# Kernel tuning notes

Measured on AMD Instinct MI355X. Metric: run time of the kernel, lower is better.

Reference implementation:

```python
import jax, jax.numpy as jnp
import numpy as np

# 3x3 Gaussian smoothing kernel (symmetric, so correlation == convolution)
GAUSS = jnp.array([[1., 2., 1.], [2., 4., 2.], [1., 2., 1.]], dtype=jnp.float32) / 16.0


def _per_sample_conv_valid(x, k):
    """Per-sample 3x3 cross-correlation. x: [B,H,W], k: [B,3,3] -> [B,H-2,W-2].

    Implemented as a grouped conv treating batch as channels (groups=B),
    matching F.conv2d(pred.permute(1,0,2,3), weight=k[:,None], groups=B).
    """
    B = x.shape[0]
    out = jax.lax.conv_general_dilated(
        x[None],            # [1, B, H, W]
        k[:, None],         # [B, 1, 3, 3]
        window_strides=(1, 1), padding='VALID',
        dimension_numbers=('NCHW', 'OIHW', 'NCHW'),
        feature_group_count=B)
    return out[0]


def _gauss_blur_same(x):
    """SAME-padded 3x3 Gaussian smoothing. x: [B,h,w] -> [B,h,w]."""
    out = jax.lax.conv_general_dilated(
        x[:, None],                 # [B,1,h,w]
        GAUSS[None, None],          # [1,1,3,3]
        window_strides=(1, 1), padding='SAME',
        dimension_numbers=('NCHW', 'OIHW', 'NCHW'))
    return out[:, 0]


def setup_inputs() -> dict:
    key = jax.random.key(0)
    k1, k2, k3, k4 = jax.random.split(key, 4)
    B, H, W = 256, 256, 256
    pred = jax.random.normal(k1, (B, H, W), dtype=jnp.float32)
    rhs = jax.random.normal(k2, (B, H - 2, W - 2), dtype=jnp.float32)
    Laplace_kernel = jax.random.normal(k3, (B, 3, 3), dtype=jnp.float32)
    Df_dr_kernel = jax.random.normal(k4, (B, 3, 3), dtype=jnp.float32)
    RR = jnp.arange(B * H * W, dtype=jnp.float32).reshape(B, H, W)
    ZZ = jnp.arange(B * H * W, dtype=jnp.float32).reshape(B, H, W)
    return {"pred": pred, "rhs": rhs, "Laplace_kernel": Laplace_kernel,
            "Df_dr_kernel": Df_dr_kernel, "RR": RR, "ZZ": ZZ}


def reference(pred, rhs, Laplace_kernel, Df_dr_kernel, RR, ZZ):
    # Finite-difference Grad-Shafranov operator (per-sample stencils).
    Lpsi = _per_sample_conv_valid(pred, Laplace_kernel)          # [B,H-2,W-2]
    Dpsi_dr = -_per_sample_conv_valid(pred, Df_dr_kernel)        # [B,H-2,W-2]
    RR_in = RR[:, 1:-1, 1:-1]
    Dpsi_dr = Dpsi_dr / RR_in
    GS_ope = Lpsi - Dpsi_dr

    # Grid spacings and normalization alfa / (hr^2 * hz^2)
    hr = RR[:, 1, 2] - RR[:, 1, 1]                               # [B]
    hz = ZZ[:, 2, 1] - ZZ[:, 1, 1]                               # [B]
    alfa = -2.0 * (hr ** 2 + hz ** 2)
    scale = (alfa / (hr ** 2 * hz ** 2))[:, None, None]
    GS_ope = GS_ope * scale

    # Gaussian smoothing then MSE against rhs
    GS_ope = _gauss_blur_same(GS_ope)
    return jnp.mean((GS_ope - rhs) ** 2)
```

## Files before the change

kernel.cpp:

```cpp
#include <hip/hip_runtime.h>

#define HW 256
#define OW 254
#define RSTRIP 16
#define NBLOCK 1024
#define NOUT (256.0f * 254.0f * 254.0f)

__device__ __forceinline__ void load_row8(const float* __restrict__ base, int row,
                                          int cL, int c0, int cB, float* p) {
    p[0] = base[row * HW + cL];
    float4 v0 = *(const float4*)&base[row * HW + c0];
    p[1] = v0.x; p[2] = v0.y; p[3] = v0.z; p[4] = v0.w;
    float4 v1 = *(const float4*)&base[row * HW + cB];
    p[5] = v1.x; p[6] = v1.y; p[7] = v1.z;
}

__global__ __launch_bounds__(256) void pde_loss_main(
    const float* __restrict__ pred, const float* __restrict__ rhs,
    const float* __restrict__ Lk,   const float* __restrict__ Dk,
    const float* __restrict__ RR,   const float* __restrict__ ZZ,
    float* __restrict__ partial)
{
    const int tid  = threadIdx.x;
    const int lane = tid & 63;
    const int wv   = tid >> 6;
    const int gw   = blockIdx.x * 4 + wv;
    const int b    = gw >> 4;
    const int strip= gw & 15;
    const int r0   = strip * RSTRIP;
    const int r1   = min(r0 + RSTRIP, OW);

    const float* predb = pred + (size_t)b * (HW * HW);
    const float* RRb   = RR   + (size_t)b * (HW * HW);
    const float* ZZb   = ZZ   + (size_t)b * (HW * HW);
    const float* rhsb  = rhs  + (size_t)b * (OW * OW);

    float kl[9], kd[9];
    #pragma unroll
    for (int q = 0; q < 9; q++) { kl[q] = Lk[b * 9 + q]; kd[q] = Dk[b * 9 + q]; }
    float hr = RRb[1 * HW + 2] - RRb[1 * HW + 1];
    float hz = ZZb[2 * HW + 1] - ZZb[1 * HW + 1];
    float hr2 = hr * hr, hz2 = hz * hz;
    const float scale = (-2.0f * (hr2 + hz2)) / (hr2 * hz2);

    const int c0 = lane * 4;
    const int cL = max(c0 - 1, 0);
    const int cB = min(c0 + 4, HW - 4);

    float pA[8], pB[8], pC[8];
    const int pa = max(r0 - 1, 0);
    load_row8(predb, pa,     cL, c0, cB, pA);
    load_row8(predb, pa + 1, cL, c0, cB, pB);

    float P[4] = {0, 0, 0, 0};
    float Q[4] = {0, 0, 0, 0};
    float acc = 0.0f;

    for (int g = r0 - 1; g <= r1; ++g) {
        float gs[6] = {0, 0, 0, 0, 0, 0};
        if (g >= 0 && g < OW) {
            load_row8(predb, g + 2, cL, c0, cB, pC);
            float rq[6];
            float4 q0 = *(const float4*)&RRb[(g + 1) * HW + c0];
            rq[0] = q0.x; rq[1] = q0.y; rq[2] = q0.z; rq[3] = q0.w;
            float2 q1 = *(const float2*)&RRb[(g + 1) * HW + c0 + 4];
            rq[4] = q1.x; rq[5] = q1.y;

            #pragma unroll
            for (int u = 0; u < 6; ++u) {
                int x = c0 - 1 + u;
                if (x >= 0 && x < OW) {
                    float sL = 0.0f, sD = 0.0f;
                    #pragma unroll
                    for (int kx = 0; kx < 3; ++kx) {
                        sL = fmaf(pA[u + kx], kl[kx],     sL);
                        sL = fmaf(pB[u + kx], kl[3 + kx], sL);
                        sL = fmaf(pC[u + kx], kl[6 + kx], sL);
                        sD = fmaf(pA[u + kx], kd[kx],     sD);
                        sD = fmaf(pB[u + kx], kd[3 + kx], sD);
                        sD = fmaf(pC[u + kx], kd[6 + kx], sD);
                    }
                    gs[u] = scale * fmaf(sD, __builtin_amdgcn_rcpf(rq[u]), sL);
                }
            }
            #pragma unroll
            for (int t = 0; t < 8; ++t) { pA[t] = pB[t]; pB[t] = pC[t]; }
        }

        float hb[4];
        #pragma unroll
        for (int t = 0; t < 4; ++t)
            hb[t] = gs[t] + 2.0f * gs[t + 1] + gs[t + 2];

        const int i = g - 1;
        if (i >= r0) {
            #pragma unroll
            for (int t = 0; t < 4; ++t) {
                int j = c0 + t;
                if (j < OW) {
                    float F = (P[t] + hb[t]) * (1.0f / 16.0f);
                    float d = F - rhsb[i * OW + j];
                    acc = fmaf(d, d, acc);
                }
            }
        }
        #pragma unroll
        for (int t = 0; t < 4; ++t) {
            P[t] = Q[t] + 2.0f * hb[t];
            Q[t] = hb[t];
        }
    }

    #pragma unroll
    for (int off = 32; off > 0; off >>= 1)
        acc += __shfl_down(acc, off, 64);
    __shared__ float sw[4];
    if (lane == 0) sw[wv] = acc;
    __syncthreads();
    if (tid == 0)
        partial[blockIdx.x] = sw[0] + sw[1] + sw[2] + sw[3];
}

__global__ __launch_bounds__(256) void pde_loss_reduce(
    const float* __restrict__ partial, int n, float* __restrict__ out)
{
    float acc = 0.0f;
    for (int i = threadIdx.x; i < n; i += 256) acc += partial[i];
    #pragma unroll
    for (int off = 32; off > 0; off >>= 1)
        acc += __shfl_down(acc, off, 64);
    __shared__ float sw[4];
    if ((threadIdx.x & 63) == 0) sw[threadIdx.x >> 6] = acc;
    __syncthreads();
    if (threadIdx.x == 0)
        out[0] = (sw[0] + sw[1] + sw[2] + sw[3]) / NOUT;
}

extern "C" void kernel_launch(void* const* d_in, const int* in_sizes, int n_in,
                              void* d_out, int out_size, void* d_ws, size_t ws_size,
                              hipStream_t stream) {
    const float* pred = (const float*)d_in[0];
    const float* rhs  = (const float*)d_in[1];
    const float* Lk   = (const float*)d_in[2];
    const float* Dk   = (const float*)d_in[3];
    const float* RR   = (const float*)d_in[4];
    const float* ZZ   = (const float*)d_in[5];
    float* out = (float*)d_out;
    float* partial = (float*)d_ws;

    pde_loss_main<<<NBLOCK, 256, 0, stream>>>(pred, rhs, Lk, Dk, RR, ZZ, partial);
    pde_loss_reduce<<<1, 256, 0, stream>>>(partial, NBLOCK, out);
}
```

Measured before the change: 238.4 us.

## Prefetch next-row pred/RR/rhs loads and halve row strips

Software-pipelines the row loop by loading the next pred row, RR row and rhs row one iteration ahead into registers, so global-load latency can overlap the stencil arithmetic. Branches inside the loop are replaced with clamped addresses and predicated selects. Strips shrink from 16 to 8 rows with twice the blocks for more parallelism, and per-sample coefficients are forced into scalar registers via readfirstlane. The costs are more registers and a larger relative halo overhead per strip.

Result: no change. 236.1 us (-0.9%).

```diff
diff --git a/kernel.cpp b/kernel.cpp
--- a/kernel.cpp
+++ b/kernel.cpp
@@ -2,8 +2,8 @@
 
 #define HW 256
 #define OW 254
-#define RSTRIP 16
-#define NBLOCK 1024
+#define RSTRIP 8
+#define NBLOCK 2048
 #define NOUT (256.0f * 254.0f * 254.0f)
 
 __device__ __forceinline__ void load_row8(const float* __restrict__ base, int row,
@@ -13,6 +13,25 @@
     p[1] = v0.x; p[2] = v0.y; p[3] = v0.z; p[4] = v0.w;
     float4 v1 = *(const float4*)&base[row * HW + cB];
     p[5] = v1.x; p[6] = v1.y; p[7] = v1.z;
+}
+
+__device__ __forceinline__ void load_rr6(const float* __restrict__ RRb, int row,
+                                         int c0, float* rq) {
+    float4 q0 = *(const float4*)&RRb[row * HW + c0];
+    rq[0] = q0.x; rq[1] = q0.y; rq[2] = q0.z; rq[3] = q0.w;
+    float2 q1 = *(const float2*)&RRb[row * HW + c0 + 4];
+    rq[4] = q1.x; rq[5] = q1.y;
+}
+
+__device__ __forceinline__ void load_rhs4(const float* __restrict__ rhsb, int row,
+                                          int c0, float* rh) {
+    #pragma unroll
+    for (int t = 0; t < 4; ++t)
+        rh[t] = rhsb[row * OW + min(c0 + t, OW - 1)];
+}
+
+__device__ __forceinline__ float uniformf(float x) {
+    return __int_as_float(__builtin_amdgcn_readfirstlane(__float_as_int(x)));
 }
 
 __global__ __launch_bounds__(256) void pde_loss_main(
@@ -25,8 +44,8 @@
     const int lane = tid & 63;
     const int wv   = tid >> 6;
     const int gw   = blockIdx.x * 4 + wv;
-    const int b    = gw >> 4;
-    const int strip= gw & 15;
+    const int b    = gw >> 5;
+    const int strip= gw & 31;
     const int r0   = strip * RSTRIP;
     const int r1   = min(r0 + RSTRIP, OW);
 
@@ -37,54 +56,54 @@
 
     float kl[9], kd[9];
     #pragma unroll
-    for (int q = 0; q < 9; q++) { kl[q] = Lk[b * 9 + q]; kd[q] = Dk[b * 9 + q]; }
+    for (int q = 0; q < 9; q++) {
+        kl[q] = uniformf(Lk[b * 9 + q]);
+        kd[q] = uniformf(Dk[b * 9 + q]);
+    }
     float hr = RRb[1 * HW + 2] - RRb[1 * HW + 1];
     float hz = ZZb[2 * HW + 1] - ZZb[1 * HW + 1];
     float hr2 = hr * hr, hz2 = hz * hz;
-    const float scale = (-2.0f * (hr2 + hz2)) / (hr2 * hz2);
+    const float scale = uniformf((-2.0f * (hr2 + hz2)) / (hr2 * hz2));
 
     const int c0 = lane * 4;
     const int cL = max(c0 - 1, 0);
     const int cB = min(c0 + 4, HW - 4);
 
-    float pA[8], pB[8], pC[8];
-    const int pa = max(r0 - 1, 0);
-    load_row8(predb, pa,     cL, c0, cB, pA);
-    load_row8(predb, pa + 1, cL, c0, cB, pB);
+    float pA[8], pB[8], pC[8], pN[8];
+    float rq[6], rqN[6], rh[4], rhN[4];
+
+    load_row8(predb, max(r0 - 1, 0), cL, c0, cB, pA);
+    load_row8(predb, r0,             cL, c0, cB, pB);
+    load_row8(predb, r0 + 1,         cL, c0, cB, pC);
+    load_rr6 (RRb,  min(max(r0, 1), HW - 2), c0, rq);
+    load_rhs4(rhsb, max(r0 - 2, 0), c0, rh);
 
     float P[4] = {0, 0, 0, 0};
     float Q[4] = {0, 0, 0, 0};
     float acc = 0.0f;
 
     for (int g = r0 - 1; g <= r1; ++g) {
-        float gs[6] = {0, 0, 0, 0, 0, 0};
-        if (g >= 0 && g < OW) {
-            load_row8(predb, g + 2, cL, c0, cB, pC);
-            float rq[6];
-            float4 q0 = *(const float4*)&RRb[(g + 1) * HW + c0];
-            rq[0] = q0.x; rq[1] = q0.y; rq[2] = q0.z; rq[3] = q0.w;
-            float2 q1 = *(const float2*)&RRb[(g + 1) * HW + c0 + 4];
-            rq[4] = q1.x; rq[5] = q1.y;
+        load_row8(predb, min(g + 3, HW - 1), cL, c0, cB, pN);
+        load_rr6 (RRb,  min(max(g + 2, 1), HW - 2), c0, rqN);
+        load_rhs4(rhsb, min(max(g, 0), OW - 1), c0, rhN);
 
+        const bool rowok = (g >= 0) && (g < OW);
+        float gs[6];
+        #pragma unroll
+        for (int u = 0; u < 6; ++u) {
+            float sL = 0.0f, sD = 0.0f;
             #pragma unroll
-            for (int u = 0; u < 6; ++u) {
-                int x = c0 - 1 + u;
-                if (x >= 0 && x < OW) {
-                    float sL = 0.0f, sD = 0.0f;
-                    #pragma unroll
-                    for (int kx = 0; kx < 3; ++kx) {
-                        sL = fmaf(pA[u + kx], kl[kx],     sL);
-                        sL = fmaf(pB[u + kx], kl[3 + kx], sL);
-                        sL = fmaf(pC[u + kx], kl[6 + kx], sL);
-                        sD = fmaf(pA[u + kx], kd[kx],     sD);
-                        sD = fmaf(pB[u + kx], kd[3 + kx], sD);
-                        sD = fmaf(pC[u + kx], kd[6 + kx], sD);
-                    }
-                    gs[u] = scale * fmaf(sD, __builtin_amdgcn_rcpf(rq[u]), sL);
-                }
+            for (int kx = 0; kx < 3; ++kx) {
+                sL = fmaf(pA[u + kx], kl[kx],     sL);
+                sL = fmaf(pB[u + kx], kl[3 + kx], sL);
+                sL = fmaf(pC[u + kx], kl[6 + kx], sL);
+                sD = fmaf(pA[u + kx], kd[kx],     sD);
+                sD = fmaf(pB[u + kx], kd[3 + kx], sD);
+                sD = fmaf(pC[u + kx], kd[6 + kx], sD);
             }
-            #pragma unroll
-            for (int t = 0; t < 8; ++t) { pA[t] = pB[t]; pB[t] = pC[t]; }
+            float gval = scale * fmaf(sD, __builtin_amdgcn_rcpf(rq[u]), sL);
+            int x = c0 - 1 + u;
+            gs[u] = (rowok && x >= 0 && x < OW) ? gval : 0.0f;
         }
 
         float hb[4];
@@ -93,19 +112,21 @@
             hb[t] = gs[t] + 2.0f * gs[t + 1] + gs[t + 2];
 
         const int i = g - 1;
-        if (i >= r0) {
-            #pragma unroll
-            for (int t = 0; t < 4; ++t) {
-                int j = c0 + t;
-                if (j < OW) {
-                    float F = (P[t] + hb[t]) * (1.0f / 16.0f);
-                    float d = F - rhsb[i * OW + j];
-                    acc = fmaf(d, d, acc);
-                }
-            }
-        }
+        const bool iok = (i >= r0);
         #pragma unroll
         for (int t = 0; t < 4; ++t) {
+            float F = (P[t] + hb[t]) * (1.0f / 16.0f);
+            float d = F - rh[t];
+            acc += (iok && (c0 + t) < OW) ? d * d : 0.0f;
+        }
+
+        #pragma unroll
+        for (int t = 0; t < 8; ++t) { pA[t] = pB[t]; pB[t] = pC[t]; pC[t] = pN[t]; }
+        #pragma unroll
+        for (int u = 0; u < 6; ++u) rq[u] = rqN[u];
+        #pragma unroll
+        for (int t = 0; t < 4; ++t) {
+            rh[t] = rhN[t];
             P[t] = Q[t] + 2.0f * hb[t];
             Q[t] = hb[t];
         }
```
